# Performance work log

Hardware: AMD Instinct MI355X
Metric: run time of the kernel (lower is better)

## Reference

```python
import jax, jax.numpy as jnp
import numpy as np

NQ = 4
DIM = 1 << NQ  # 16 statevector amplitudes

def _cnot_perm(c, t):
    idx = np.arange(DIM)
    cbit = (idx >> (NQ - 1 - c)) & 1
    return np.where(cbit == 1, idx ^ (1 << (NQ - 1 - t)), idx)

# BasicEntanglerLayers CNOT ring: (0,1),(1,2),(2,3),(3,0)
CNOT_PERMS = [jnp.asarray(_cnot_perm(q, (q + 1) % NQ)) for q in range(NQ)]
_idx = np.arange(DIM)
SIGNS = jnp.asarray(np.stack([1.0 - 2.0 * ((_idx >> (NQ - 1 - q)) & 1) for q in range(NQ)]).astype(np.float32))  # (NQ, DIM), PauliZ eigenvalues


def _apply_rx(state, theta, q):
    """Apply RX(theta) on wire q. state: (N, DIM) complex64. theta: scalar or (N,)."""
    half = theta * 0.5
    c = jnp.cos(half).astype(jnp.complex64)
    js = (1j * jnp.sin(half)).astype(jnp.complex64)
    if jnp.ndim(theta) == 1:
        c = c[:, None, None]
        js = js[:, None, None]
    d1, d2 = 1 << q, 1 << (NQ - 1 - q)
    st = state.reshape(-1, d1, 2, d2)
    a0, a1 = st[:, :, 0, :], st[:, :, 1, :]
    out = jnp.stack([c * a0 - js * a1, c * a1 - js * a0], axis=2)
    return out.reshape(state.shape)


def circuit(angles, weights):
    """AngleEmbedding(RX) + BasicEntanglerLayers(RX + CNOT ring) + <Z_i>.
    angles: (N, NQ) real. weights: (L, NQ). returns (N, NQ)."""
    N = angles.shape[0]
    state = jnp.zeros((N, DIM), jnp.complex64).at[:, 0].set(1.0)
    for q in range(NQ):  # AngleEmbedding: per-sample RX angles
        state = _apply_rx(state, angles[:, q], q)
    for l in range(weights.shape[0]):  # entangler layers (static count)
        for q in range(NQ):
            state = _apply_rx(state, weights[l, q], q)
        for q in range(NQ):
            state = state[:, CNOT_PERMS[q]]
    probs = jnp.real(state) ** 2 + jnp.imag(state) ** 2
    return probs @ SIGNS.T


def setup_inputs() -> dict:
    key = jax.random.key(0)
    ks = jax.random.split(key, 5)
    B, S = 32, 2048
    TWO_PI = 6.2831853
    return {
        "x": jax.random.normal(ks[0], (B, S, NQ), jnp.float32),
        "weights_Q": jax.random.uniform(ks[1], (1, NQ), jnp.float32) * TWO_PI,
        "weights_K": jax.random.uniform(ks[2], (1, NQ), jnp.float32) * TWO_PI,
        "weights_V": jax.random.uniform(ks[3], (1, NQ), jnp.float32) * TWO_PI,
        "weights_C": jax.random.uniform(ks[4], (1, NQ), jnp.float32) * TWO_PI,
    }


def reference(x, weights_Q, weights_K, weights_V, weights_C):
    B, S, E = x.shape  # E == NQ == 4
    flat = x.reshape(B * S, E)
    Q = circuit(flat, weights_Q).reshape(B, S, E)
    K = circuit(flat, weights_K).reshape(B, S, E)
    V = circuit(flat, weights_V).reshape(B, S, E)
    scores = jnp.einsum('bqe,bke->bqk', Q, K) / (E ** 0.5)
    attn = jax.nn.softmax(scores, axis=-1)
    ctx = jnp.einsum('bqk,bke->bqe', attn, V)
    return circuit(ctx.reshape(B * S, E), weights_C).reshape(B, S, E)
```

## Files before the change

### kernel.cpp

```cpp
#include <hip/hip_runtime.h>

#define DIM 16
#define SEQ 2048
#define CHUNK 64
#define NPAIR (CHUNK / 2)
#define NCHUNK 32
#define RPT 4

typedef float v2f __attribute__((ext_vector_type(2)));
typedef float v4f __attribute__((ext_vector_type(4)));

static __device__ __forceinline__ float fexp2(float x) {
#if __has_builtin(__builtin_amdgcn_exp2f)
    return __builtin_amdgcn_exp2f(x);
#else
    return exp2f(x);
#endif
}


template<int P>
__device__ __forceinline__ void rx_bit(float sr[DIM], float si[DIM], float ch, float sh) {
    constexpr int m = 1 << P;
    #pragma unroll
    for (int i = 0; i < DIM; ++i) {
        if ((i & m) == 0) {
            const int j = i | m;
            float r0 = sr[i], i0 = si[i], r1 = sr[j], i1 = si[j];
            sr[i] = fmaf(ch, r0,  sh * i1);
            si[i] = fmaf(ch, i0, -sh * r1);
            sr[j] = fmaf(ch, r1,  sh * i0);
            si[j] = fmaf(ch, i1, -sh * r0);
        }
    }
}

template<int PC, int PT>
__device__ __forceinline__ void cnot_g(float sr[DIM], float si[DIM]) {
    constexpr int cm = 1 << PC, tm = 1 << PT;
    #pragma unroll
    for (int i = 0; i < DIM; ++i) {
        if ((i & cm) && !(i & tm)) {
            const int j = i | tm;
            float t;
            t = sr[i]; sr[i] = sr[j]; sr[j] = t;
            t = si[i]; si[i] = si[j]; si[j] = t;
        }
    }
}

__device__ __forceinline__ void embed(float sr[DIM], float si[DIM], float4 a) {
    float c0, s0, c1, s1, c2, s2, c3, s3;
    __sincosf(0.5f * a.x, &s0, &c0);
    __sincosf(0.5f * a.y, &s1, &c1);
    __sincosf(0.5f * a.z, &s2, &c2);
    __sincosf(0.5f * a.w, &s3, &c3);
    float A[4] = {c0 * c1, c0 * s1, s0 * c1, s0 * s1};
    float B[4] = {c2 * c3, c2 * s3, s2 * c3, s2 * s3};
    #pragma unroll
    for (int idx = 0; idx < DIM; ++idx) {
        const float p = A[idx >> 2] * B[idx & 3];
        const int m = __builtin_popcount(idx) & 3;
        sr[idx] = (m == 0) ? p : (m == 2) ? -p : 0.f;
        si[idx] = (m == 1) ? -p : (m == 3) ? p : 0.f;
    }
}

__device__ __forceinline__ void layer(float sr[DIM], float si[DIM], float4 w) {
    float ch, sh;
    __sincosf(0.5f * w.x, &sh, &ch); rx_bit<3>(sr, si, ch, sh);
    __sincosf(0.5f * w.y, &sh, &ch); rx_bit<2>(sr, si, ch, sh);
    __sincosf(0.5f * w.z, &sh, &ch); rx_bit<1>(sr, si, ch, sh);
    __sincosf(0.5f * w.w, &sh, &ch); rx_bit<0>(sr, si, ch, sh);
    cnot_g<3,2>(sr, si);
    cnot_g<2,1>(sr, si);
    cnot_g<1,0>(sr, si);
    cnot_g<0,3>(sr, si);
}

__device__ __forceinline__ float4 measure(const float sr[DIM], const float si[DIM]) {
    float e0 = 0.f, e1 = 0.f, e2 = 0.f, e3 = 0.f;
    #pragma unroll
    for (int i = 0; i < DIM; ++i) {
        float p = fmaf(sr[i], sr[i], si[i] * si[i]);
        e0 += (i & 8) ? -p : p;
        e1 += (i & 4) ? -p : p;
        e2 += (i & 2) ? -p : p;
        e3 += (i & 1) ? -p : p;
    }
    return make_float4(e0, e1, e2, e3);
}


__global__ __launch_bounds__(256) void qkv_kernel(
        const float* __restrict__ x,
        const float* __restrict__ wQp, const float* __restrict__ wKp,
        const float* __restrict__ wVp,
        float4* __restrict__ Q, float* __restrict__ Kt, float* __restrict__ Vt) {
    const int i = blockIdx.x * 256 + threadIdx.x;
    const int which = blockIdx.y;
    const float4 xv = ((const float4*)x)[i];
    const float* wp = (which == 0) ? wQp : (which == 1) ? wKp : wVp;
    const float4 w = *(const float4*)wp;

    float sr[DIM], si[DIM];
    embed(sr, si, xv);
    layer(sr, si, w);
    const float4 r = measure(sr, si);

    if (which == 0) {
        Q[i] = r;
    } else {
        const int bb = i >> 11, rr = i & (SEQ - 1);
        const int p = rr >> 1, h = rr & 1;
        float* base = ((which == 1) ? Kt : Vt)
                      + ((size_t)bb * (SEQ / 2) + p) * 8 + h;
        base[0] = r.x; base[2] = r.y; base[4] = r.z; base[6] = r.w;
    }
}


__global__ __launch_bounds__(256, 4) void attn_partial(
        const v4f* __restrict__ Q, const float* __restrict__ Kt,
        const float* __restrict__ Vt,
        float* __restrict__ pden, v4f* __restrict__ pctx, int n) {
    __shared__ v4f vs[2 * NPAIR];

    const int rg = blockIdx.x;
    const int c  = blockIdx.y;
    const int b  = rg >> 1;

    const v4f* Vtc = (const v4f*)(Vt + ((size_t)b * (SEQ / 2) + c * NPAIR) * 8);
    if (threadIdx.x < 2 * NPAIR)
        vs[threadIdx.x] = Vtc[threadIdx.x];
    __syncthreads();

    const float SC = 0.72134752044f;
    const int row0 = rg * (256 * RPT) + threadIdx.x;

    v2f qx[RPT], qy[RPT], qz[RPT], qw[RPT];
    #pragma unroll
    for (int j = 0; j < RPT; ++j) {
        const v4f q = Q[row0 + j * 256];
        qx[j] = (v2f){q.x * SC, q.x * SC};
        qy[j] = (v2f){q.y * SC, q.y * SC};
        qz[j] = (v2f){q.z * SC, q.z * SC};
        qw[j] = (v2f){q.w * SC, q.w * SC};
    }

    v2f den[RPT], ax[RPT], ay[RPT], az[RPT], aw[RPT];
    #pragma unroll
    for (int j = 0; j < RPT; ++j) {
        den[j] = (v2f){0.f, 0.f};
        ax[j] = den[j]; ay[j] = den[j]; az[j] = den[j]; aw[j] = den[j];
    }

    const v4f* Ktc = (const v4f*)(Kt + ((size_t)b * (SEQ / 2) + c * NPAIR) * 8);

    #pragma unroll 4
    for (int p = 0; p < NPAIR; ++p) {
        const v4f kAB = Ktc[2 * p + 0];
        const v4f kCD = Ktc[2 * p + 1];
        const v2f kx = kAB.xy, ky = kAB.zw, kz = kCD.xy, kw = kCD.zw;
        const v4f vA = vs[2 * p + 0];
        const v4f vB = vs[2 * p + 1];
        const v2f vx = vA.xy, vy = vA.zw, vz = vB.xy, vw = vB.zw;
        #pragma unroll
        for (int j = 0; j < RPT; ++j) {
            v2f s = __builtin_elementwise_fma(qy[j], ky, qx[j] * kx);
            s     = __builtin_elementwise_fma(qz[j], kz, s);
            s     = __builtin_elementwise_fma(qw[j], kw, s);
            const v2f e = (v2f){fexp2(s.x), fexp2(s.y)};
            den[j] += e;
            ax[j] = __builtin_elementwise_fma(e, vx, ax[j]);
            ay[j] = __builtin_elementwise_fma(e, vy, ay[j]);
            az[j] = __builtin_elementwise_fma(e, vz, az[j]);
            aw[j] = __builtin_elementwise_fma(e, vw, aw[j]);
        }
    }

    #pragma unroll
    for (int j = 0; j < RPT; ++j) {
        const int row = row0 + j * 256;
        __builtin_nontemporal_store(den[j].x + den[j].y, pden + ((size_t)c * n + row));
        const v4f ct = (v4f){ax[j].x + ax[j].y, ay[j].x + ay[j].y,
                             az[j].x + az[j].y, aw[j].x + aw[j].y};
        __builtin_nontemporal_store(ct, pctx + ((size_t)c * n + row));
    }
}


__global__ __launch_bounds__(256) void combine_kernel(
        const float* __restrict__ pden, const v4f* __restrict__ pctx,
        const float* __restrict__ wCp, float4* __restrict__ out, int n) {
    const int row = blockIdx.x * 256 + threadIdx.x;

    float d = 0.f;
    float c0 = 0.f, c1 = 0.f, c2 = 0.f, c3 = 0.f;
    #pragma unroll 8
    for (int c = 0; c < NCHUNK; ++c) {
        d += __builtin_nontemporal_load(pden + ((size_t)c * n + row));
        const v4f p = __builtin_nontemporal_load(pctx + ((size_t)c * n + row));
        c0 += p.x; c1 += p.y; c2 += p.z; c3 += p.w;
    }
    const float inv = 1.0f / d;
    const float4 ctx = make_float4(c0 * inv, c1 * inv, c2 * inv, c3 * inv);

    const float4 wC = *(const float4*)wCp;
    float sr[DIM], si[DIM];
    embed(sr, si, ctx);
    layer(sr, si, wC);
    out[row] = measure(sr, si);
}


extern "C" void kernel_launch(void* const* d_in, const int* in_sizes, int n_in,
                              void* d_out, int out_size, void* d_ws, size_t ws_size,
                              hipStream_t stream) {
    const float* x  = (const float*)d_in[0];
    const float* wQ = (const float*)d_in[1];
    const float* wK = (const float*)d_in[2];
    const float* wV = (const float*)d_in[3];
    const float* wC = (const float*)d_in[4];

    const int n = in_sizes[0] / 4;
    float4* Q    = (float4*)d_ws;
    float*  Kt   = (float*)(Q + n);
    float*  Vt   = Kt + 4 * n;
    v4f*   pctx  = (v4f*)(Vt + 4 * n);
    float* pden  = (float*)(pctx + (size_t)NCHUNK * n);

    dim3 qgrid(n / 256, 3);
    qkv_kernel<<<qgrid, 256, 0, stream>>>(x, wQ, wK, wV, Q, Kt, Vt);

    dim3 agrid(n / (256 * RPT), NCHUNK);
    attn_partial<<<agrid, 256, 0, stream>>>((const v4f*)Q, Kt, Vt,
                                            pden, pctx, n);

    combine_kernel<<<n / 256, 256, 0, stream>>>(pden, pctx, wC, (float4*)d_out, n);
}
```

Baseline: 106.0 us.

## Interleave K and V pairs, drop LDS staging, halve chunk count

K and V are now stored interleaved in one buffer, so each key pair's K and V values sit in one 64-byte record. The attention kernel reads V directly from global memory (uniform, cached loads) instead of staging it in shared memory behind a barrier. Chunk size doubles and the chunk count halves, which halves the partial-sum traffic and the combine kernel's reduction work but also halves the attention grid size, leaving fewer blocks to spread across the GPU. The unroll factor is also reduced to keep register use in check.

```diff
diff --git a/kernel.cpp b/kernel.cpp
--- a/kernel.cpp
+++ b/kernel.cpp
@@ -2,9 +2,9 @@
 
 #define DIM 16
 #define SEQ 2048
-#define CHUNK 64
+#define CHUNK 128
 #define NPAIR (CHUNK / 2)
-#define NCHUNK 32
+#define NCHUNK 16
 #define RPT 4
 
 typedef float v2f __attribute__((ext_vector_type(2)));
@@ -96,7 +96,7 @@
         const float* __restrict__ x,
         const float* __restrict__ wQp, const float* __restrict__ wKp,
         const float* __restrict__ wVp,
-        float4* __restrict__ Q, float* __restrict__ Kt, float* __restrict__ Vt) {
+        float4* __restrict__ Q, float* __restrict__ KVt) {
     const int i = blockIdx.x * 256 + threadIdx.x;
     const int which = blockIdx.y;
     const float4 xv = ((const float4*)x)[i];
@@ -113,27 +113,19 @@
     } else {
         const int bb = i >> 11, rr = i & (SEQ - 1);
         const int p = rr >> 1, h = rr & 1;
-        float* base = ((which == 1) ? Kt : Vt)
-                      + ((size_t)bb * (SEQ / 2) + p) * 8 + h;
+        float* base = KVt + ((size_t)bb * (SEQ / 2) + p) * 16 + h
+                      + ((which == 2) ? 8 : 0);
         base[0] = r.x; base[2] = r.y; base[4] = r.z; base[6] = r.w;
     }
 }
 
 
 __global__ __launch_bounds__(256, 4) void attn_partial(
-        const v4f* __restrict__ Q, const float* __restrict__ Kt,
-        const float* __restrict__ Vt,
+        const v4f* __restrict__ Q, const float* __restrict__ KVt,
         float* __restrict__ pden, v4f* __restrict__ pctx, int n) {
-    __shared__ v4f vs[2 * NPAIR];
-
     const int rg = blockIdx.x;
     const int c  = blockIdx.y;
     const int b  = rg >> 1;
-
-    const v4f* Vtc = (const v4f*)(Vt + ((size_t)b * (SEQ / 2) + c * NPAIR) * 8);
-    if (threadIdx.x < 2 * NPAIR)
-        vs[threadIdx.x] = Vtc[threadIdx.x];
-    __syncthreads();
 
     const float SC = 0.72134752044f;
     const int row0 = rg * (256 * RPT) + threadIdx.x;
@@ -155,16 +147,16 @@
         ax[j] = den[j]; ay[j] = den[j]; az[j] = den[j]; aw[j] = den[j];
     }
 
-    const v4f* Ktc = (const v4f*)(Kt + ((size_t)b * (SEQ / 2) + c * NPAIR) * 8);
-
-    #pragma unroll 4
+    const v4f* KVc = (const v4f*)(KVt + ((size_t)b * (SEQ / 2) + c * NPAIR) * 16);
+
+    #pragma unroll 2
     for (int p = 0; p < NPAIR; ++p) {
-        const v4f kAB = Ktc[2 * p + 0];
-        const v4f kCD = Ktc[2 * p + 1];
+        const v4f kAB = KVc[4 * p + 0];
+        const v4f kCD = KVc[4 * p + 1];
+        const v4f vAB = KVc[4 * p + 2];
+        const v4f vCD = KVc[4 * p + 3];
         const v2f kx = kAB.xy, ky = kAB.zw, kz = kCD.xy, kw = kCD.zw;
-        const v4f vA = vs[2 * p + 0];
-        const v4f vB = vs[2 * p + 1];
-        const v2f vx = vA.xy, vy = vA.zw, vz = vB.xy, vw = vB.zw;
+        const v2f vx = vAB.xy, vy = vAB.zw, vz = vCD.xy, vw = vCD.zw;
         #pragma unroll
         for (int j = 0; j < RPT; ++j) {
             v2f s = __builtin_elementwise_fma(qy[j], ky, qx[j] * kx);
@@ -225,16 +217,15 @@
 
     const int n = in_sizes[0] / 4;
     float4* Q    = (float4*)d_ws;
-    float*  Kt   = (float*)(Q + n);
-    float*  Vt   = Kt + 4 * n;
-    v4f*   pctx  = (v4f*)(Vt + 4 * n);
+    float*  KVt  = (float*)(Q + n);
+    v4f*   pctx  = (v4f*)(KVt + 8 * n);
     float* pden  = (float*)(pctx + (size_t)NCHUNK * n);
 
     dim3 qgrid(n / 256, 3);
-    qkv_kernel<<<qgrid, 256, 0, stream>>>(x, wQ, wK, wV, Q, Kt, Vt);
+    qkv_kernel<<<qgrid, 256, 0, stream>>>(x, wQ, wK, wV, Q, KVt);
 
     dim3 agrid(n / (256 * RPT), NCHUNK);
-    attn_partial<<<agrid, 256, 0, stream>>>((const v4f*)Q, Kt, Vt,
+    attn_partial<<<agrid, 256, 0, stream>>>((const v4f*)Q, KVt,
                                             pden, pctx, n);
 
     combine_kernel<<<n / 256, 256, 0, stream>>>(pden, pctx, wC, (float4*)d_out, n);
```

New measurement: 104.5 us. No clear change (-1.4%).
